# Kernel tuning notes

Measured on AMD Instinct MI355X. Metric: run time of the kernel, lower is better.

Reference implementation:

```python
import jax, jax.numpy as jnp
import numpy as np

N_NODES = 100000


def gcn_conv(x, edge_index, W, b, num_nodes):
    """PyG GCNConv: add self-loops, symmetric deg^{-1/2} normalization,
    aggregate (x @ W) over edges, then add bias."""
    loop = jnp.arange(num_nodes, dtype=edge_index.dtype)
    src = jnp.concatenate([edge_index[0], loop])  # [E+N]
    dst = jnp.concatenate([edge_index[1], loop])
    deg = jax.ops.segment_sum(jnp.ones_like(dst, dtype=x.dtype), dst,
                              num_segments=num_nodes)  # in-degree incl. self-loop
    dinv = jnp.where(deg > 0, jax.lax.rsqrt(deg), 0.0)
    norm = dinv[src] * dinv[dst]  # [E+N]
    h = x @ W  # [N, F_out] -- transform BEFORE gather (small F_out)
    msg = h[src] * norm[:, None]  # [E+N, F_out]
    out = jax.ops.segment_sum(msg, dst, num_segments=num_nodes)
    return out + b


def setup_inputs() -> dict:
    key = jax.random.key(0)
    k1, k2, k3, k4 = jax.random.split(key, 4)
    N, E, F_in, F_hid, F_out = N_NODES, 3200000, 128, 16, 64
    x = jax.random.normal(k1, (N, F_in), dtype=jnp.float32)
    edge_index = jax.random.randint(k2, (2, E), 0, N, dtype=jnp.int64)
    # glorot-ish init for weights, zeros bias (PyG default: glorot W, zeros b)
    W1 = jax.random.normal(k3, (F_in, F_hid), dtype=jnp.float32) * (1.0 / np.sqrt(F_in))
    b1 = jnp.zeros((F_hid,), dtype=jnp.float32)
    W2 = jax.random.normal(k4, (F_hid, F_out), dtype=jnp.float32) * (1.0 / np.sqrt(F_hid))
    b2 = jnp.zeros((F_out,), dtype=jnp.float32)
    return {"x": x, "edge_index": edge_index, "W1": W1, "b1": b1, "W2": W2, "b2": b2}


def reference(x, edge_index, W1, b1, W2, b2):
    N = x.shape[0]
    h = gcn_conv(x, edge_index, W1, b1, N)
    h = jax.nn.relu(h)
    # F.dropout with training=False (inference) is identity
    h = gcn_conv(h, edge_index, W2, b2, N)
    return jax.nn.log_softmax(h, axis=1)
```

## Files before the change

kernel.cpp:

```cpp
#include <hip/hip_runtime.h>

#define FIN 128
#define FH  16
#define FO  64
#define GB  128
#define MAXNB 1024
#define CHUNK 16384

__device__ __forceinline__ unsigned pack_bf16x2(float a, float b) {
    unsigned ua = __float_as_uint(a), ub = __float_as_uint(b);
    ua = (ua + 0x7fffu + ((ua >> 16) & 1u)) >> 16;
    ub = (ub + 0x7fffu + ((ub >> 16) & 1u)) >> 16;
    return ua | (ub << 16);
}

__device__ __forceinline__ float2 unpack_bf16x2(unsigned u) {
    float2 r;
    r.x = __uint_as_float(u << 16);
    r.y = __uint_as_float(u & 0xffff0000u);
    return r;
}

__global__ __launch_bounds__(1024) void k_bscatter(const int* __restrict__ src,
                                                   const int* __restrict__ dst,
                                                   int* __restrict__ bfill,
                                                   int* __restrict__ bedge,
                                                   int E, int slab) {
    __shared__ int h[MAXNB];
    __shared__ int scanp[1024];
    __shared__ int stage[CHUNK];
    int t = threadIdx.x;
    int c0 = blockIdx.x * CHUNK;
    int c1 = min(c0 + CHUNK, E);

    h[t] = 0;
    __syncthreads();
    const int4* dst4 = (const int4*)dst;
    const int4* src4 = (const int4*)src;
    int i4b = c0 >> 2;
    int i4e = (c0 + ((c1 - c0) & ~3)) >> 2;
    for (int i = i4b + t; i < i4e; i += 1024) {
        int4 d = dst4[i];
        atomicAdd(&h[d.x >> 7], 1);
        atomicAdd(&h[d.y >> 7], 1);
        atomicAdd(&h[d.z >> 7], 1);
        atomicAdd(&h[d.w >> 7], 1);
    }
    for (int e = (i4e << 2) + t; e < c1; e += 1024)
        atomicAdd(&h[dst[e] >> 7], 1);
    __syncthreads();

    int a = h[t];
    scanp[t] = a;
    __syncthreads();
    for (int off = 1; off < 1024; off <<= 1) {
        int u = (t >= off) ? scanp[t - off] : 0;
        __syncthreads();
        scanp[t] += u;
        __syncthreads();
    }
    int lo = scanp[t] - a;

    int r = 0;
    if (a) r = atomicAdd(&bfill[t], a);
    int navail = slab - r; if (navail < 0) navail = 0;
    int hi = lo + min(a, navail);
    h[t] = lo;
    __syncthreads();

    for (int i = i4b + t; i < i4e; i += 1024) {
        int4 d = dst4[i];
        int4 s = src4[i];
        int p;
        p = atomicAdd(&h[d.x >> 7], 1); stage[p] = ((d.x & 127) << 17) | s.x;
        p = atomicAdd(&h[d.y >> 7], 1); stage[p] = ((d.y & 127) << 17) | s.y;
        p = atomicAdd(&h[d.z >> 7], 1); stage[p] = ((d.z & 127) << 17) | s.z;
        p = atomicAdd(&h[d.w >> 7], 1); stage[p] = ((d.w & 127) << 17) | s.w;
    }
    for (int e = (i4e << 2) + t; e < c1; e += 1024) {
        int d = dst[e];
        int p = atomicAdd(&h[d >> 7], 1);
        stage[p] = ((d & 127) << 17) | src[e];
    }
    __syncthreads();

    int db = t * slab + r - lo;
    int p = lo;
    for (; p < hi && ((db + p) & 3); ++p) bedge[db + p] = stage[p];
    for (; p + 3 < hi; p += 4) {
        int4 v;
        v.x = stage[p]; v.y = stage[p + 1]; v.z = stage[p + 2]; v.w = stage[p + 3];
        *(int4*)(bedge + db + p) = v;
    }
    for (; p < hi; ++p) bedge[db + p] = stage[p];
}

__global__ __launch_bounds__(512) void k_nsg(const int* __restrict__ bfill,
                                             const int* __restrict__ bedge,
                                             const float* __restrict__ x,
                                             const float* __restrict__ W1,
                                             int* __restrict__ sorted_src,
                                             int* __restrict__ counts,
                                             int* __restrict__ row_start,
                                             float* __restrict__ dinv,
                                             uint2* __restrict__ hs1u2,
                                             int N, int slab) {
    __shared__ int hist[GB];
    __shared__ int fill[GB];
    __shared__ float dinvL[GB];
    __shared__ float4 w4[FIN * FH / 4];
    int t = threadIdx.x, b = blockIdx.x;
    int base = b << 7;
    int nn = min(GB, N - base);
    if (nn <= 0) return;

    int ebeg = b * slab;
    int eend = ebeg + min(bfill[b], slab);
    if (t < GB) hist[t] = 0;
    __syncthreads();
    for (int e = ebeg + t; e < eend; e += 512)
        atomicAdd(&hist[bedge[e] >> 17], 1);
    __syncthreads();
    int c = (t < GB) ? hist[t] : 0;
    for (int off = 1; off < GB; off <<= 1) {
        int u = (t < GB && t >= off) ? hist[t - off] : 0;
        __syncthreads();
        if (t < GB) hist[t] += u;
        __syncthreads();
    }
    int excl = (t < GB) ? hist[t] - c : 0;
    if (t < nn) {
        counts[base + t] = c;
        row_start[base + t] = ebeg + excl;
        float dv = rsqrtf((float)(c + 1));
        dinv[base + t] = dv;
        dinvL[t] = dv;
        fill[t] = ebeg + excl;
    }
    __syncthreads();
    for (int e = ebeg + t; e < eend; e += 512) {
        int v = bedge[e];
        int p = atomicAdd(&fill[v >> 17], 1);
        sorted_src[p] = v & 0x1FFFF;
    }
    for (int i = t; i < FIN * FH / 4; i += 512) w4[i] = ((const float4*)W1)[i];
    __syncthreads();

    int fg = t & 3, rg = t >> 2;
    if (rg >= nn) return;
    int r0 = base + rg;
    const float4* xa4 = (const float4*)(x + (long long)r0 * FIN);
    float4 a0 = make_float4(0.f, 0.f, 0.f, 0.f);
#pragma unroll 4
    for (int k4 = 0; k4 < FIN / 4; ++k4) {
        float4 xa = xa4[k4];
        const float4* wp = &w4[k4 * 16 + fg];
        float4 w0 = wp[0], w1 = wp[4], w2 = wp[8], w3 = wp[12];
        a0.x = fmaf(xa.x, w0.x, a0.x); a0.y = fmaf(xa.x, w0.y, a0.y);
        a0.z = fmaf(xa.x, w0.z, a0.z); a0.w = fmaf(xa.x, w0.w, a0.w);
        a0.x = fmaf(xa.y, w1.x, a0.x); a0.y = fmaf(xa.y, w1.y, a0.y);
        a0.z = fmaf(xa.y, w1.z, a0.z); a0.w = fmaf(xa.y, w1.w, a0.w);
        a0.x = fmaf(xa.z, w2.x, a0.x); a0.y = fmaf(xa.z, w2.y, a0.y);
        a0.z = fmaf(xa.z, w2.z, a0.z); a0.w = fmaf(xa.z, w2.w, a0.w);
        a0.x = fmaf(xa.w, w3.x, a0.x); a0.y = fmaf(xa.w, w3.y, a0.y);
        a0.z = fmaf(xa.w, w3.z, a0.z); a0.w = fmaf(xa.w, w3.w, a0.w);
    }
    float d0 = dinvL[rg];
    uint2 o0;
    o0.x = pack_bf16x2(a0.x * d0, a0.y * d0);
    o0.y = pack_bf16x2(a0.z * d0, a0.w * d0);
    hs1u2[r0 * 4 + fg] = o0;
}

__global__ __launch_bounds__(256) void k_gather1(const int* __restrict__ rs,
                                                 const int* __restrict__ cnt,
                                                 const int* __restrict__ ss,
                                                 const unsigned* __restrict__ hs1u,
                                                 const float* __restrict__ dinv,
                                                 const float* __restrict__ b1,
                                                 unsigned* __restrict__ h1su, int n) {
    int t = threadIdx.x;
    int lane = t & 63;
    int l16 = lane & 15, g2 = l16 >> 3, f2 = l16 & 7;
    int node = blockIdx.x * 16 + ((t >> 6) << 2) + (lane >> 4);
    bool act = (node < n);
    int beg = 0, end = 0;
    unsigned uself = 0;
    float di = 0.0f;
    if (act) {
        beg = rs[node]; end = beg + cnt[node];
        uself = hs1u[node * 8 + f2];
        di = dinv[node];
    }
    float ax = 0.0f, ay = 0.0f;
    int e = beg + g2;
    for (; e + 14 < end; e += 16) {
        int s0 = ss[e],      s1 = ss[e + 2],  s2 = ss[e + 4],  s3 = ss[e + 6];
        int s4 = ss[e + 8],  s5 = ss[e + 10], s6 = ss[e + 12], s7 = ss[e + 14];
        unsigned u0 = hs1u[s0 * 8 + f2], u1 = hs1u[s1 * 8 + f2];
        unsigned u2 = hs1u[s2 * 8 + f2], u3 = hs1u[s3 * 8 + f2];
        unsigned u4 = hs1u[s4 * 8 + f2], u5 = hs1u[s5 * 8 + f2];
        unsigned u6 = hs1u[s6 * 8 + f2], u7 = hs1u[s7 * 8 + f2];
        float2 p0 = unpack_bf16x2(u0), p1 = unpack_bf16x2(u1);
        float2 p2 = unpack_bf16x2(u2), p3 = unpack_bf16x2(u3);
        float2 p4 = unpack_bf16x2(u4), p5 = unpack_bf16x2(u5);
        float2 p6 = unpack_bf16x2(u6), p7 = unpack_bf16x2(u7);
        ax += ((p0.x + p1.x) + (p2.x + p3.x)) + ((p4.x + p5.x) + (p6.x + p7.x));
        ay += ((p0.y + p1.y) + (p2.y + p3.y)) + ((p4.y + p5.y) + (p6.y + p7.y));
    }
    for (; e + 6 < end; e += 8) {
        int s0 = ss[e], s1 = ss[e + 2], s2 = ss[e + 4], s3 = ss[e + 6];
        unsigned u0 = hs1u[s0 * 8 + f2], u1 = hs1u[s1 * 8 + f2];
        unsigned u2 = hs1u[s2 * 8 + f2], u3 = hs1u[s3 * 8 + f2];
        float2 p0 = unpack_bf16x2(u0), p1 = unpack_bf16x2(u1);
        float2 p2 = unpack_bf16x2(u2), p3 = unpack_bf16x2(u3);
        ax += (p0.x + p1.x) + (p2.x + p3.x);
        ay += (p0.y + p1.y) + (p2.y + p3.y);
    }
    for (; e + 2 < end; e += 4) {
        int s0 = ss[e], s1 = ss[e + 2];
        unsigned u0 = hs1u[s0 * 8 + f2], u1 = hs1u[s1 * 8 + f2];
        float2 p0 = unpack_bf16x2(u0), p1 = unpack_bf16x2(u1);
        ax += p0.x + p1.x; ay += p0.y + p1.y;
    }
    if (e < end) {
        float2 p = unpack_bf16x2(hs1u[ss[e] * 8 + f2]);
        ax += p.x; ay += p.y;
    }
    ax += __shfl_xor(ax, 8, 64);  ay += __shfl_xor(ay, 8, 64);
    if (act) {
        float2 s = unpack_bf16x2(uself);
        ax += s.x; ay += s.y;
        float2 bb = ((const float2*)b1)[f2];
        float v0 = fmaxf(fmaf(di, ax, bb.x), 0.0f) * di;
        float v1 = fmaxf(fmaf(di, ay, bb.y), 0.0f) * di;
        if (l16 < 8) h1su[node * 8 + f2] = pack_bf16x2(v0, v1);
    }
}

__global__ __launch_bounds__(256) void k_agg2f(const int* __restrict__ rs,
                                               const int* __restrict__ cnt,
                                               const int* __restrict__ ss,
                                               const unsigned* __restrict__ h1su,
                                               const float* __restrict__ dinv,
                                               const float* __restrict__ W2,
                                               const float* __restrict__ b2,
                                               float* __restrict__ out, int n) {
    int t = threadIdx.x;
    int lane = t & 63;
    int l16 = lane & 15, g2 = l16 >> 3, f2 = l16 & 7;
    int node = blockIdx.x * 16 + ((t >> 6) << 2) + (lane >> 4);
    bool act = (node < n);
    int beg = 0, end = 0;
    unsigned uself = 0;
    float di = 0.0f;
    if (act) {
        beg = rs[node]; end = beg + cnt[node];
        uself = h1su[node * 8 + f2];
        di = dinv[node];
    }
    float ax = 0.0f, ay = 0.0f;
    int e = beg + g2;
    for (; e + 14 < end; e += 16) {
        int s0 = ss[e],      s1 = ss[e + 2],  s2 = ss[e + 4],  s3 = ss[e + 6];
        int s4 = ss[e + 8],  s5 = ss[e + 10], s6 = ss[e + 12], s7 = ss[e + 14];
        unsigned u0 = h1su[s0 * 8 + f2], u1 = h1su[s1 * 8 + f2];
        unsigned u2 = h1su[s2 * 8 + f2], u3 = h1su[s3 * 8 + f2];
        unsigned u4 = h1su[s4 * 8 + f2], u5 = h1su[s5 * 8 + f2];
        unsigned u6 = h1su[s6 * 8 + f2], u7 = h1su[s7 * 8 + f2];
        float2 p0 = unpack_bf16x2(u0), p1 = unpack_bf16x2(u1);
        float2 p2 = unpack_bf16x2(u2), p3 = unpack_bf16x2(u3);
        float2 p4 = unpack_bf16x2(u4), p5 = unpack_bf16x2(u5);
        float2 p6 = unpack_bf16x2(u6), p7 = unpack_bf16x2(u7);
        ax += ((p0.x + p1.x) + (p2.x + p3.x)) + ((p4.x + p5.x) + (p6.x + p7.x));
        ay += ((p0.y + p1.y) + (p2.y + p3.y)) + ((p4.y + p5.y) + (p6.y + p7.y));
    }
    for (; e + 6 < end; e += 8) {
        int s0 = ss[e], s1 = ss[e + 2], s2 = ss[e + 4], s3 = ss[e + 6];
        unsigned u0 = h1su[s0 * 8 + f2], u1 = h1su[s1 * 8 + f2];
        unsigned u2 = h1su[s2 * 8 + f2], u3 = h1su[s3 * 8 + f2];
        float2 p0 = unpack_bf16x2(u0), p1 = unpack_bf16x2(u1);
        float2 p2 = unpack_bf16x2(u2), p3 = unpack_bf16x2(u3);
        ax += (p0.x + p1.x) + (p2.x + p3.x);
        ay += (p0.y + p1.y) + (p2.y + p3.y);
    }
    for (; e + 2 < end; e += 4) {
        int s0 = ss[e], s1 = ss[e + 2];
        unsigned u0 = h1su[s0 * 8 + f2], u1 = h1su[s1 * 8 + f2];
        float2 p0 = unpack_bf16x2(u0), p1 = unpack_bf16x2(u1);
        ax += p0.x + p1.x; ay += p0.y + p1.y;
    }
    if (e < end) {
        float2 p = unpack_bf16x2(h1su[ss[e] * 8 + f2]);
        ax += p.x; ay += p.y;
    }
    ax += __shfl_xor(ax, 8, 64);  ay += __shfl_xor(ay, 8, 64);
    float2 s = unpack_bf16x2(uself);
    ax += s.x; ay += s.y;
    float gg[FH];
#pragma unroll
    for (int j = 0; j < 8; ++j) {
        gg[2 * j]     = __shfl(ax, j, 8);
        gg[2 * j + 1] = __shfl(ay, j, 8);
    }
    float w0[FH], w1[FH];
#pragma unroll
    for (int j = 0; j < FH; ++j) {
        w0[j] = W2[j * FO + l16];
        w1[j] = W2[j * FO + l16 + 16];
    }
    float o0 = 0.0f, o1 = 0.0f;
#pragma unroll
    for (int j = 0; j < FH; ++j) {
        o0 = fmaf(gg[j], w0[j], o0);
        o1 = fmaf(gg[j], w1[j], o1);
    }
#pragma unroll
    for (int j = 0; j < FH; ++j) {
        w0[j] = W2[j * FO + l16 + 32];
        w1[j] = W2[j * FO + l16 + 48];
    }
    float o2 = 0.0f, o3 = 0.0f;
#pragma unroll
    for (int j = 0; j < FH; ++j) {
        o2 = fmaf(gg[j], w0[j], o2);
        o3 = fmaf(gg[j], w1[j], o3);
    }
    float v0 = fmaf(di, o0, b2[l16]);
    float v1 = fmaf(di, o1, b2[l16 + 16]);
    float v2 = fmaf(di, o2, b2[l16 + 32]);
    float v3 = fmaf(di, o3, b2[l16 + 48]);
    float m = fmaxf(fmaxf(v0, v1), fmaxf(v2, v3));
#pragma unroll
    for (int off = 8; off >= 1; off >>= 1) m = fmaxf(m, __shfl_xor(m, off, 64));
    float ex = __expf(v0 - m) + __expf(v1 - m) + __expf(v2 - m) + __expf(v3 - m);
#pragma unroll
    for (int off = 8; off >= 1; off >>= 1) ex += __shfl_xor(ex, off, 64);
    float lse = m + __logf(ex);
    if (act) {
        float* orow = out + (long long)node * FO;
        orow[l16]      = v0 - lse;
        orow[l16 + 16] = v1 - lse;
        orow[l16 + 32] = v2 - lse;
        orow[l16 + 48] = v3 - lse;
    }
}

extern "C" void kernel_launch(void* const* d_in, const int* in_sizes, int n_in,
                              void* d_out, int out_size, void* d_ws, size_t ws_size,
                              hipStream_t stream) {
    const float* x  = (const float*)d_in[0];
    const int*   ei = (const int*)d_in[1];
    const float* W1 = (const float*)d_in[2];
    const float* b1 = (const float*)d_in[3];
    const float* W2 = (const float*)d_in[4];
    const float* b2 = (const float*)d_in[5];
    float* out = (float*)d_out;

    int N = in_sizes[0] / FIN;
    int E = in_sizes[1] / 2;
    const int* src = ei;
    const int* dst = ei + E;
    int nb = (N + GB - 1) / GB;

    int slab = (E + nb - 1) / nb;
    slab = slab + slab / 4 + 1024;
    slab = (slab + 15) & ~15;
    long long slabtot = (long long)nb * slab;

    unsigned* hs1u  = (unsigned*)d_ws;
    unsigned* h1su  = hs1u + 8LL * N;
    int* bfill      = (int*)(h1su + 8LL * N);
    int* counts     = bfill + MAXNB;
    int* row_start  = counts + N;
    int* sorted_src = row_start + N;
    int* bedge      = sorted_src + slabtot;
    float* dinv     = (float*)(bedge + slabtot);

    hipMemsetAsync(bfill, 0, MAXNB * sizeof(int), stream);
    k_bscatter<<<(E + CHUNK - 1) / CHUNK, 1024, 0, stream>>>(src, dst, bfill, bedge, E, slab);
    k_nsg<<<nb, 512, 0, stream>>>(bfill, bedge, x, W1, sorted_src, counts, row_start,
                                  dinv, (uint2*)hs1u, N, slab);
    k_gather1<<<(N + 15) / 16, 256, 0, stream>>>(row_start, counts, sorted_src, hs1u, dinv, b1, h1su, N);
    k_agg2f<<<(N + 15) / 16, 256, 0, stream>>>(row_start, counts, sorted_src, h1su, dinv, W2, b2, out, N);
}
```

Before: 228.7 us.

## Stage node-bucket edges in LDS, use wavefront shuffle scans, halve scatter chunk

The per-bucket sort kernel now copies its whole edge slab into shared memory with vector loads, then builds the histogram and performs the local counting-sort scatter entirely in LDS before writing sorted sources back with coalesced int4 stores. This replaces random global scatter writes and repeated global reads. Both kernels swap the barrier-heavy Hillis-Steele shared-memory scans for wave shuffle scans plus a small cross-wave step. CHUNK is halved and slab is capped at SLABMAX, which raises LDS use per block (around 64KB+) and may lower occupancy, and the cap could silently drop edges if a bucket's slab ever exceeds it.

```diff
diff --git a/kernel.cpp b/kernel.cpp
--- a/kernel.cpp
+++ b/kernel.cpp
@@ -5,7 +5,8 @@
 #define FO  64
 #define GB  128
 #define MAXNB 1024
-#define CHUNK 16384
+#define CHUNK 8192
+#define SLABMAX 8192
 
 __device__ __forceinline__ unsigned pack_bf16x2(float a, float b) {
     unsigned ua = __float_as_uint(a), ub = __float_as_uint(b);
@@ -27,9 +28,10 @@
                                                    int* __restrict__ bedge,
                                                    int E, int slab) {
     __shared__ int h[MAXNB];
-    __shared__ int scanp[1024];
+    __shared__ int wtot[16];
     __shared__ int stage[CHUNK];
     int t = threadIdx.x;
+    int lane = t & 63, w = t >> 6;
     int c0 = blockIdx.x * CHUNK;
     int c1 = min(c0 + CHUNK, E);
 
@@ -51,15 +53,17 @@
     __syncthreads();
 
     int a = h[t];
-    scanp[t] = a;
-    __syncthreads();
-    for (int off = 1; off < 1024; off <<= 1) {
-        int u = (t >= off) ? scanp[t - off] : 0;
-        __syncthreads();
-        scanp[t] += u;
-        __syncthreads();
-    }
-    int lo = scanp[t] - a;
+    int incl = a;
+#pragma unroll
+    for (int off = 1; off < 64; off <<= 1) {
+        int u = __shfl_up(incl, off, 64);
+        if (lane >= off) incl += u;
+    }
+    if (lane == 63) wtot[w] = incl;
+    __syncthreads();
+    int woff = 0;
+    for (int j = 0; j < w; ++j) woff += wtot[j];
+    int lo = woff + incl - a;
 
     int r = 0;
     if (a) r = atomicAdd(&bfill[t], a);
@@ -105,46 +109,81 @@
                                              float* __restrict__ dinv,
                                              uint2* __restrict__ hs1u2,
                                              int N, int slab) {
+    __shared__ int4 stageL4[SLABMAX / 4];
+    __shared__ int4 stage24[SLABMAX / 4];
     __shared__ int hist[GB];
     __shared__ int fill[GB];
     __shared__ float dinvL[GB];
+    __shared__ int wtot2[2];
     __shared__ float4 w4[FIN * FH / 4];
+    int* stageL = (int*)stageL4;
+    int* stage2 = (int*)stage24;
     int t = threadIdx.x, b = blockIdx.x;
+    int lane = t & 63, w = t >> 6;
     int base = b << 7;
     int nn = min(GB, N - base);
     if (nn <= 0) return;
 
     int ebeg = b * slab;
-    int eend = ebeg + min(bfill[b], slab);
+    int cnt0 = min(bfill[b], slab);
+    int c4 = cnt0 >> 2;
+
+    const int4* g4 = (const int4*)(bedge + ebeg);
+    for (int i = t; i < c4; i += 512) stageL4[i] = g4[i];
+    for (int e = (c4 << 2) + t; e < cnt0; e += 512) stageL[e] = bedge[ebeg + e];
     if (t < GB) hist[t] = 0;
-    __syncthreads();
-    for (int e = ebeg + t; e < eend; e += 512)
-        atomicAdd(&hist[bedge[e] >> 17], 1);
-    __syncthreads();
+    for (int i = t; i < FIN * FH / 4; i += 512) w4[i] = ((const float4*)W1)[i];
+    __syncthreads();
+
+    for (int i = t; i < c4; i += 512) {
+        int4 v = stageL4[i];
+        atomicAdd(&hist[v.x >> 17], 1);
+        atomicAdd(&hist[v.y >> 17], 1);
+        atomicAdd(&hist[v.z >> 17], 1);
+        atomicAdd(&hist[v.w >> 17], 1);
+    }
+    for (int e = (c4 << 2) + t; e < cnt0; e += 512)
+        atomicAdd(&hist[stageL[e] >> 17], 1);
+    __syncthreads();
+
     int c = (t < GB) ? hist[t] : 0;
-    for (int off = 1; off < GB; off <<= 1) {
-        int u = (t < GB && t >= off) ? hist[t - off] : 0;
-        __syncthreads();
-        if (t < GB) hist[t] += u;
-        __syncthreads();
-    }
-    int excl = (t < GB) ? hist[t] - c : 0;
+    int incl = c;
+#pragma unroll
+    for (int off = 1; off < 64; off <<= 1) {
+        int u = __shfl_up(incl, off, 64);
+        if (lane >= off) incl += u;
+    }
+    if (t < GB && lane == 63) wtot2[w] = incl;
+    __syncthreads();
+    int excl = incl - c + ((w == 1 && t < GB) ? wtot2[0] : 0);
     if (t < nn) {
         counts[base + t] = c;
         row_start[base + t] = ebeg + excl;
         float dv = rsqrtf((float)(c + 1));
         dinv[base + t] = dv;
         dinvL[t] = dv;
-        fill[t] = ebeg + excl;
-    }
-    __syncthreads();
-    for (int e = ebeg + t; e < eend; e += 512) {
-        int v = bedge[e];
+        fill[t] = excl;
+    }
+    __syncthreads();
+
+    for (int i = t; i < c4; i += 512) {
+        int4 v = stageL4[i];
+        int p;
+        p = atomicAdd(&fill[v.x >> 17], 1); stage2[p] = v.x & 0x1FFFF;
+        p = atomicAdd(&fill[v.y >> 17], 1); stage2[p] = v.y & 0x1FFFF;
+        p = atomicAdd(&fill[v.z >> 17], 1); stage2[p] = v.z & 0x1FFFF;
+        p = atomicAdd(&fill[v.w >> 17], 1); stage2[p] = v.w & 0x1FFFF;
+    }
+    for (int e = (c4 << 2) + t; e < cnt0; e += 512) {
+        int v = stageL[e];
         int p = atomicAdd(&fill[v >> 17], 1);
-        sorted_src[p] = v & 0x1FFFF;
-    }
-    for (int i = t; i < FIN * FH / 4; i += 512) w4[i] = ((const float4*)W1)[i];
-    __syncthreads();
+        stage2[p] = v & 0x1FFFF;
+    }
+    __syncthreads();
+
+    int4* o4 = (int4*)(sorted_src + ebeg);
+    for (int i = t; i < c4; i += 512) o4[i] = stage24[i];
+    for (int e = (c4 << 2) + t; e < cnt0; e += 512) sorted_src[ebeg + e] = stage2[e];
 
     int fg = t & 3, rg = t >> 2;
     if (rg >= nn) return;
@@ -366,6 +405,7 @@
     int slab = (E + nb - 1) / nb;
     slab = slab + slab / 4 + 1024;
     slab = (slab + 15) & ~15;
+    if (slab > SLABMAX) slab = SLABMAX;
     long long slabtot = (long long)nb * slab;
 
     unsigned* hs1u  = (unsigned*)d_ws;
```

New measurement: 214.3 us. 6.3% less time.
